# Optimization experiments

Hardware: AMD Instinct MI355X
Metric: run time of the kernel (lower is better)

The kernel has to match this reference:

```python
import jax, jax.numpy as jnp
import numpy as np
from jax import lax

B, T, K = 1024, 512, 32


def setup_inputs() -> dict:
    key = jax.random.key(0)
    k1, k2, k3 = jax.random.split(key, 3)
    labels = jax.random.randint(k1, (B, T), 0, K, dtype=jnp.int32)
    y_pred = jax.random.normal(k2, (B, T, K), dtype=jnp.float32)
    # glorot-uniform-ish transition matrix
    limit = np.sqrt(6.0 / (K + K)).astype(np.float32)
    trans = jax.random.uniform(k3, (K, K), minval=-limit, maxval=limit, dtype=jnp.float32)
    mask = jnp.ones((B, T), dtype=jnp.float32)
    return {"labels": labels, "y_pred": y_pred, "trans": trans, "mask": mask}


def crf_loss(labels, y_pred, trans, mask):
    n_tags = trans.shape[0]
    y_true = jax.nn.one_hot(labels, n_tags, dtype=y_pred.dtype)  # [B,T,K]
    y_true = y_true * mask[:, :, None]  # sequence_masking with value 0

    # --- target path score ---
    point_score = jnp.einsum('bni,bni->b', y_true, y_pred)
    trans_score = jnp.einsum('bni,ij,bnj->b', y_true[:, :-1], trans, y_true[:, 1:])
    target = point_score + trans_score

    # --- log partition via forward algorithm (logsumexp scan) ---
    alpha0 = y_pred[:, 0]  # [B,K]

    def step(alpha, xs):
        emit, m = xs  # emit: [B,K], m: [B,1]
        new = jax.nn.logsumexp(alpha[:, :, None] + trans[None], axis=1) + emit
        alpha = m * new + (1.0 - m) * alpha
        return alpha, None

    xs = (jnp.swapaxes(y_pred[:, 1:], 0, 1),          # [T-1,B,K]
          jnp.swapaxes(mask[:, 1:, None], 0, 1))      # [T-1,B,1]
    alpha, _ = lax.scan(step, alpha0, xs)
    log_norm = jax.nn.logsumexp(alpha, axis=1)  # [B]
    return log_norm - target


def reference(labels, y_pred, trans, mask):
    return crf_loss(labels, y_pred, trans, mask)
```

## Files before the change

### kernel.cpp

```cpp
#include <hip/hip_runtime.h>


#define K32 32
#define Tt  512
#define NCH 4
#define CHL 128
#define NSEG 2

typedef float  float4v __attribute__((ext_vector_type(4)));
typedef short  short8v __attribute__((ext_vector_type(8)));

__device__ inline float bf2f_lo(unsigned d) { return __uint_as_float(d << 16); }
__device__ inline float bf2f_hi(unsigned d) { return __uint_as_float(d & 0xFFFF0000u); }

__device__ inline unsigned pack_trunc(float hi, float lo) {
    return __builtin_amdgcn_perm(__float_as_uint(hi), __float_as_uint(lo), 0x07060302u);
}
__device__ inline unsigned short f2bf_rne(float x) {
    unsigned u = __float_as_uint(x);
    return (unsigned short)((u + 0x7FFFu + ((u >> 16) & 1u)) >> 16);
}

union F8 { unsigned u[4]; short8v v; };

__global__ __launch_bounds__(256, 4) void crf_chunk(
    const int*   __restrict__ labels,
    const float* __restrict__ y_pred,
    const float* __restrict__ trans,
    const float* __restrict__ mask,
    unsigned*    __restrict__ wsMT,
    float*       __restrict__ wsS,
    float*       __restrict__ wsSc)
{
    __shared__ float expAll[4][64 * 32];

    const int lane = threadIdx.x & 63;
    const int wv   = __builtin_amdgcn_readfirstlane(threadIdx.x >> 6);
    const int gw   = blockIdx.x * 4 + wv;
    const int n    = lane & 15;
    const int q    = lane >> 4;
    const int seq  = gw >> 2;
    const int c    = gw & 3;

    float* eb = &expAll[wv][0];

    const float* yp  = y_pred + (size_t)seq * Tt * K32;
    const int*   lb  = labels + (size_t)seq * Tt;
    const float* mkp = mask   + (size_t)seq * Tt;
    const int tbase = c * CHL;

    float4 pre[8];
    {
        const float4* gs = (const float4*)(yp + (size_t)tbase * K32);
#pragma unroll
        for (int jj = 0; jj < 8; ++jj) pre[jj] = gs[jj * 64 + lane];
    }

    unsigned long long mb[NSEG];
    float sc = 0.0f;
#pragma unroll
    for (int s = 0; s < NSEG; ++s) {
        const int t = tbase + s * 64 + lane;
        const int lab0 = lb[t];
        const float mlane = mkp[t];
        float scl = yp[t * K32 + lab0] * mlane;
        if (t < Tt - 1) {
            scl += trans[lab0 * K32 + lb[t + 1]] * (mlane * mkp[t + 1]);
        }
        sc += scl;
        mb[s] = __ballot(mlane != 0.0f);
    }
    if (c == 0) mb[0] &= ~1ull;
#pragma unroll
    for (int s = 1; s < 64; s <<= 1) sc += __shfl_xor(sc, s, 64);

    F8 AE0, AE1;
#pragma unroll
    for (int h = 0; h < 4; ++h) {
        const int k0 = (h < 2) ? (q * 4 + 2 * h) : (16 + q * 4 + 2 * (h - 2));
        const int k1 = k0 + 1;
        AE0.u[h] = ((unsigned)f2bf_rne(__expf(trans[k0 * K32 + n]) * 0.03125f)) |
                   (((unsigned)f2bf_rne(__expf(trans[k1 * K32 + n]) * 0.03125f)) << 16);
        AE1.u[h] = ((unsigned)f2bf_rne(__expf(trans[k0 * K32 + 16 + n]) * 0.03125f)) |
                   (((unsigned)f2bf_rne(__expf(trans[k1 * K32 + 16 + n]) * 0.03125f)) << 16);
    }

    F8 B0, B1;
#pragma unroll
    for (int h = 0; h < 4; ++h) {
        const int r0 = (h < 2) ? (q * 4 + 2 * h) : (16 + q * 4 + 2 * (h - 2));
        const int r1 = r0 + 1;
        unsigned w0 = 0, w1 = 0;
        if (r0 == n)      w0 |= 0x3F80u;
        if (r1 == n)      w0 |= 0x3F800000u;
        if (r0 == 16 + n) w1 |= 0x3F80u;
        if (r1 == 16 + n) w1 |= 0x3F800000u;
        B0.u[h] = w0;
        B1.u[h] = w1;
    }

    float Slog    = 0.0f;
    int   applied = 0;

    const int svoff0 = q * 4;
    const int svoff1 = 16 + q * 4;

    auto body = [&](int i) {
        const float4v sv0 = *(const float4v*)&eb[i * 32 + svoff0];
        const float4v sv1 = *(const float4v*)&eb[i * 32 + svoff1];

        float4v c00 = {0.f, 0.f, 0.f, 0.f}, c01 = {0.f, 0.f, 0.f, 0.f};
        float4v c10 = {0.f, 0.f, 0.f, 0.f}, c11 = {0.f, 0.f, 0.f, 0.f};
        c00 = __builtin_amdgcn_mfma_f32_16x16x32_bf16(AE0.v, B0.v, c00, 0, 0, 0);
        c01 = __builtin_amdgcn_mfma_f32_16x16x32_bf16(AE0.v, B1.v, c01, 0, 0, 0);
        c10 = __builtin_amdgcn_mfma_f32_16x16x32_bf16(AE1.v, B0.v, c10, 0, 0, 0);
        c11 = __builtin_amdgcn_mfma_f32_16x16x32_bf16(AE1.v, B1.v, c11, 0, 0, 0);

        c00 *= sv0; c01 *= sv0; c10 *= sv1; c11 *= sv1;

        if ((applied & 7) == 7) {
            const float cn = __uint_as_float(
                __builtin_amdgcn_readfirstlane(__float_as_uint(c00[0])));
            const float rs = 1.0f / cn;
            c00 *= rs; c01 *= rs; c10 *= rs; c11 *= rs;
            Slog += __logf(cn);
        }
        ++applied;

        B0.u[0] = pack_trunc(c00[1], c00[0]);
        B0.u[1] = pack_trunc(c00[3], c00[2]);
        B0.u[2] = pack_trunc(c10[1], c10[0]);
        B0.u[3] = pack_trunc(c10[3], c10[2]);
        B1.u[0] = pack_trunc(c01[1], c01[0]);
        B1.u[1] = pack_trunc(c01[3], c01[2]);
        B1.u[2] = pack_trunc(c11[1], c11[0]);
        B1.u[3] = pack_trunc(c11[3], c11[2]);
    };

    for (int seg = 0; seg < NSEG; ++seg) {
#pragma unroll
        for (int jj = 0; jj < 8; ++jj) {
            float4v e;
            e[0] = __expf(pre[jj].x); e[1] = __expf(pre[jj].y);
            e[2] = __expf(pre[jj].z); e[3] = __expf(pre[jj].w);
            *(float4v*)&eb[(jj * 64 + lane) * 4] = e;
        }
        if (seg + 1 < NSEG) {
            const float4* gs = (const float4*)(yp + (size_t)(tbase + (seg + 1) * 64) * K32);
#pragma unroll
            for (int jj = 0; jj < 8; ++jj) pre[jj] = gs[jj * 64 + lane];
        }

        const unsigned long long mbits = mb[seg];
        if (mbits == ~0ull) {
#pragma unroll 8
            for (int i = 0; i < 64; ++i) body(i);
        } else {
#pragma unroll 4
            for (int i = 0; i < 64; ++i) {
                if ((mbits >> i) & 1ull) body(i);
            }
        }
    }

    {
        unsigned* Nd = (unsigned*)eb;
        *(uint2*)&Nd[n * 20 + q * 2]            = make_uint2(B0.u[0], B0.u[1]);
        *(uint2*)&Nd[n * 20 + 8 + q * 2]        = make_uint2(B0.u[2], B0.u[3]);
        *(uint2*)&Nd[(16 + n) * 20 + q * 2]     = make_uint2(B1.u[0], B1.u[1]);
        *(uint2*)&Nd[(16 + n) * 20 + 8 + q * 2] = make_uint2(B1.u[2], B1.u[3]);
    }
    const unsigned short* Ncm = (const unsigned short*)eb;
    unsigned* md = wsMT + (size_t)gw * 512;
    for (int idx = lane; idx < 512; idx += 64) {
        const int k = idx >> 4, d = idx & 15;
        const unsigned lo = Ncm[(2 * d) * 40 + k];
        const unsigned hi = Ncm[(2 * d + 1) * 40 + k];
        md[idx] = lo | (hi << 16);
    }
    if (lane == 0) {
        wsS[gw]  = Slog + (float)applied * 3.46573590f;
        wsSc[gw] = sc;
    }
}

__global__ __launch_bounds__(64) void crf_combine(
    const float*    __restrict__ y_pred,
    const unsigned* __restrict__ wsMT,
    const float*    __restrict__ wsS,
    const float*    __restrict__ wsSc,
    float*          __restrict__ out)
{
    const int lane = threadIdx.x;
    const int h    = lane >> 5;
    const int j    = lane & 31;
    const int seq  = blockIdx.x;

    const uint4* mb = (const uint4*)(wsMT + (size_t)seq * NCH * 512);
    uint4 mA[NCH], mB[NCH];
#pragma unroll
    for (int cc = 0; cc < NCH; ++cc) {
        mA[cc] = mb[cc * 128 + j * 4 + 2 * h];
        mB[cc] = mb[cc * 128 + j * 4 + 2 * h + 1];
    }

    const float* yp = y_pred + (size_t)seq * Tt * K32;
    const float a0 = yp[j];
    const float m0 = __shfl(a0, 0, 64);
    float p = __expf(a0 - m0);
    float S = m0;

    float scs = 0.0f;
#pragma unroll
    for (int cc = 0; cc < NCH; ++cc) {
        S   += wsS[seq * NCH + cc];
        scs += wsSc[seq * NCH + cc];
    }

    const int cb = h << 4;
#pragma unroll
    for (int cc = 0; cc < NCH; ++cc) {
        const float cn = __shfl(p, 0, 64);
        const unsigned u0 = mA[cc].x, u1 = mA[cc].y, u2 = mA[cc].z, u3 = mA[cc].w;
        const unsigned u4 = mB[cc].x, u5 = mB[cc].y, u6 = mB[cc].z, u7 = mB[cc].w;
        float acc = 0.0f;
        acc = fmaf(__shfl(p, cb +  0, 64), bf2f_lo(u0), acc);
        acc = fmaf(__shfl(p, cb +  1, 64), bf2f_hi(u0), acc);
        acc = fmaf(__shfl(p, cb +  2, 64), bf2f_lo(u1), acc);
        acc = fmaf(__shfl(p, cb +  3, 64), bf2f_hi(u1), acc);
        acc = fmaf(__shfl(p, cb +  4, 64), bf2f_lo(u2), acc);
        acc = fmaf(__shfl(p, cb +  5, 64), bf2f_hi(u2), acc);
        acc = fmaf(__shfl(p, cb +  6, 64), bf2f_lo(u3), acc);
        acc = fmaf(__shfl(p, cb +  7, 64), bf2f_hi(u3), acc);
        acc = fmaf(__shfl(p, cb +  8, 64), bf2f_lo(u4), acc);
        acc = fmaf(__shfl(p, cb +  9, 64), bf2f_hi(u4), acc);
        acc = fmaf(__shfl(p, cb + 10, 64), bf2f_lo(u5), acc);
        acc = fmaf(__shfl(p, cb + 11, 64), bf2f_hi(u5), acc);
        acc = fmaf(__shfl(p, cb + 12, 64), bf2f_lo(u6), acc);
        acc = fmaf(__shfl(p, cb + 13, 64), bf2f_hi(u6), acc);
        acc = fmaf(__shfl(p, cb + 14, 64), bf2f_lo(u7), acc);
        acc = fmaf(__shfl(p, cb + 15, 64), bf2f_hi(u7), acc);
        acc += __shfl_xor(acc, 32, 64);
        p = acc * (1.0f / cn);
        S += __logf(cn);
    }

    float sp = p;
    sp += __shfl_xor(sp,  1, 64);
    sp += __shfl_xor(sp,  2, 64);
    sp += __shfl_xor(sp,  4, 64);
    sp += __shfl_xor(sp,  8, 64);
    sp += __shfl_xor(sp, 16, 64);

    if (lane == 0) {
        out[seq] = S + __logf(sp) - scs;
    }
}

extern "C" void kernel_launch(void* const* d_in, const int* in_sizes, int n_in,
                              void* d_out, int out_size, void* d_ws, size_t ws_size,
                              hipStream_t stream) {
    const int*   labels = (const int*)  d_in[0];
    const float* y_pred = (const float*)d_in[1];
    const float* trans  = (const float*)d_in[2];
    const float* mask   = (const float*)d_in[3];
    float* out = (float*)d_out;

    unsigned* wsMT = (unsigned*)d_ws;
    float* wsS  = (float*)((char*)d_ws + (size_t)1024 * NCH * 512 * 4);
    float* wsSc = wsS + 1024 * NCH;

    crf_chunk<<<1024, 256, 0, stream>>>(labels, y_pred, trans, mask, wsMT, wsS, wsSc);
    crf_combine<<<1024, 64, 0, stream>>>(y_pred, wsMT, wsS, wsSc, out);
}
```

Measured before the change: 143.0 us.

## Fuse chunk and combine kernels via shared-memory handoff within block

Merges the chunk kernel and the combine kernel into one launch. Each block now handles a single sequence: its four waves compute the four chunk transfer matrices, write them to LDS instead of global workspace, and wave 0 chains them after a block barrier. This removes a kernel launch, the global workspace round trip and the second pass over the data. In exchange, three waves sit idle during the serial combine phase.

```diff
diff --git a/kernel.cpp b/kernel.cpp
--- a/kernel.cpp
+++ b/kernel.cpp
@@ -23,24 +23,21 @@
 
 union F8 { unsigned u[4]; short8v v; };
 
-__global__ __launch_bounds__(256, 4) void crf_chunk(
+__global__ __launch_bounds__(256, 4) void crf_fused(
     const int*   __restrict__ labels,
     const float* __restrict__ y_pred,
     const float* __restrict__ trans,
     const float* __restrict__ mask,
-    unsigned*    __restrict__ wsMT,
-    float*       __restrict__ wsS,
-    float*       __restrict__ wsSc)
+    float*       __restrict__ out)
 {
-    __shared__ float expAll[4][64 * 32];
+    __shared__ float expAll[4][2048];
 
     const int lane = threadIdx.x & 63;
     const int wv   = __builtin_amdgcn_readfirstlane(threadIdx.x >> 6);
-    const int gw   = blockIdx.x * 4 + wv;
     const int n    = lane & 15;
     const int q    = lane >> 4;
-    const int seq  = gw >> 2;
-    const int c    = gw & 3;
+    const int seq  = blockIdx.x;
+    const int c    = wv;
 
     float* eb = &expAll[wv][0];
 
@@ -164,96 +161,91 @@
     }
 
     {
-        unsigned* Nd = (unsigned*)eb;
+        unsigned* Nd = (unsigned*)eb + 1024;
         *(uint2*)&Nd[n * 20 + q * 2]            = make_uint2(B0.u[0], B0.u[1]);
         *(uint2*)&Nd[n * 20 + 8 + q * 2]        = make_uint2(B0.u[2], B0.u[3]);
         *(uint2*)&Nd[(16 + n) * 20 + q * 2]     = make_uint2(B1.u[0], B1.u[1]);
         *(uint2*)&Nd[(16 + n) * 20 + 8 + q * 2] = make_uint2(B1.u[2], B1.u[3]);
     }
-    const unsigned short* Ncm = (const unsigned short*)eb;
-    unsigned* md = wsMT + (size_t)gw * 512;
-    for (int idx = lane; idx < 512; idx += 64) {
-        const int k = idx >> 4, d = idx & 15;
-        const unsigned lo = Ncm[(2 * d) * 40 + k];
-        const unsigned hi = Ncm[(2 * d + 1) * 40 + k];
-        md[idx] = lo | (hi << 16);
+    {
+        const unsigned short* Ncm = (const unsigned short*)((unsigned*)eb + 1024);
+        unsigned* md = (unsigned*)eb;
+        for (int idx = lane; idx < 512; idx += 64) {
+            const int k = idx >> 4, d = idx & 15;
+            const unsigned lo = Ncm[(2 * d) * 40 + k];
+            const unsigned hi = Ncm[(2 * d + 1) * 40 + k];
+            md[idx] = lo | (hi << 16);
+        }
     }
     if (lane == 0) {
-        wsS[gw]  = Slog + (float)applied * 3.46573590f;
-        wsSc[gw] = sc;
-    }
-}
-
-__global__ __launch_bounds__(64) void crf_combine(
-    const float*    __restrict__ y_pred,
-    const unsigned* __restrict__ wsMT,
-    const float*    __restrict__ wsS,
-    const float*    __restrict__ wsSc,
-    float*          __restrict__ out)
-{
-    const int lane = threadIdx.x;
-    const int h    = lane >> 5;
-    const int j    = lane & 31;
-    const int seq  = blockIdx.x;
-
-    const uint4* mb = (const uint4*)(wsMT + (size_t)seq * NCH * 512);
-    uint4 mA[NCH], mB[NCH];
-#pragma unroll
-    for (int cc = 0; cc < NCH; ++cc) {
-        mA[cc] = mb[cc * 128 + j * 4 + 2 * h];
-        mB[cc] = mb[cc * 128 + j * 4 + 2 * h + 1];
-    }
-
-    const float* yp = y_pred + (size_t)seq * Tt * K32;
-    const float a0 = yp[j];
-    const float m0 = __shfl(a0, 0, 64);
-    float p = __expf(a0 - m0);
-    float S = m0;
-
-    float scs = 0.0f;
-#pragma unroll
-    for (int cc = 0; cc < NCH; ++cc) {
-        S   += wsS[seq * NCH + cc];
-        scs += wsSc[seq * NCH + cc];
-    }
-
-    const int cb = h << 4;
-#pragma unroll
-    for (int cc = 0; cc < NCH; ++cc) {
-        const float cn = __shfl(p, 0, 64);
-        const unsigned u0 = mA[cc].x, u1 = mA[cc].y, u2 = mA[cc].z, u3 = mA[cc].w;
-        const unsigned u4 = mB[cc].x, u5 = mB[cc].y, u6 = mB[cc].z, u7 = mB[cc].w;
-        float acc = 0.0f;
-        acc = fmaf(__shfl(p, cb +  0, 64), bf2f_lo(u0), acc);
-        acc = fmaf(__shfl(p, cb +  1, 64), bf2f_hi(u0), acc);
-        acc = fmaf(__shfl(p, cb +  2, 64), bf2f_lo(u1), acc);
-        acc = fmaf(__shfl(p, cb +  3, 64), bf2f_hi(u1), acc);
-        acc = fmaf(__shfl(p, cb +  4, 64), bf2f_lo(u2), acc);
-        acc = fmaf(__shfl(p, cb +  5, 64), bf2f_hi(u2), acc);
-        acc = fmaf(__shfl(p, cb +  6, 64), bf2f_lo(u3), acc);
-        acc = fmaf(__shfl(p, cb +  7, 64), bf2f_hi(u3), acc);
-        acc = fmaf(__shfl(p, cb +  8, 64), bf2f_lo(u4), acc);
-        acc = fmaf(__shfl(p, cb +  9, 64), bf2f_hi(u4), acc);
-        acc = fmaf(__shfl(p, cb + 10, 64), bf2f_lo(u5), acc);
-        acc = fmaf(__shfl(p, cb + 11, 64), bf2f_hi(u5), acc);
-        acc = fmaf(__shfl(p, cb + 12, 64), bf2f_lo(u6), acc);
-        acc = fmaf(__shfl(p, cb + 13, 64), bf2f_hi(u6), acc);
-        acc = fmaf(__shfl(p, cb + 14, 64), bf2f_lo(u7), acc);
-        acc = fmaf(__shfl(p, cb + 15, 64), bf2f_hi(u7), acc);
-        acc += __shfl_xor(acc, 32, 64);
-        p = acc * (1.0f / cn);
-        S += __logf(cn);
-    }
-
-    float sp = p;
-    sp += __shfl_xor(sp,  1, 64);
-    sp += __shfl_xor(sp,  2, 64);
-    sp += __shfl_xor(sp,  4, 64);
-    sp += __shfl_xor(sp,  8, 64);
-    sp += __shfl_xor(sp, 16, 64);
-
-    if (lane == 0) {
-        out[seq] = S + __logf(sp) - scs;
+        eb[1984] = Slog + (float)applied * 3.46573590f;
+        eb[1985] = sc;
+    }
+
+    __syncthreads();
+
+    if (wv == 0) {
+        const int h = lane >> 5;
+        const int j = lane & 31;
+
+        uint4 mA[NCH], mB[NCH];
+#pragma unroll
+        for (int cc = 0; cc < NCH; ++cc) {
+            const unsigned* mt = (const unsigned*)&expAll[cc][0];
+            mA[cc] = *(const uint4*)&mt[j * 16 + 8 * h];
+            mB[cc] = *(const uint4*)&mt[j * 16 + 8 * h + 4];
+        }
+
+        const float a0 = yp[j];
+        const float m0 = __shfl(a0, 0, 64);
+        float p = __expf(a0 - m0);
+        float S = m0;
+
+        float scs = 0.0f;
+#pragma unroll
+        for (int cc = 0; cc < NCH; ++cc) {
+            S   += expAll[cc][1984];
+            scs += expAll[cc][1985];
+        }
+
+        const int cb = h << 4;
+#pragma unroll
+        for (int cc = 0; cc < NCH; ++cc) {
+            const float cn = __shfl(p, 0, 64);
+            const unsigned u0 = mA[cc].x, u1 = mA[cc].y, u2 = mA[cc].z, u3 = mA[cc].w;
+            const unsigned u4 = mB[cc].x, u5 = mB[cc].y, u6 = mB[cc].z, u7 = mB[cc].w;
+            float acc = 0.0f;
+            acc = fmaf(__shfl(p, cb +  0, 64), bf2f_lo(u0), acc);
+            acc = fmaf(__shfl(p, cb +  1, 64), bf2f_hi(u0), acc);
+            acc = fmaf(__shfl(p, cb +  2, 64), bf2f_lo(u1), acc);
+            acc = fmaf(__shfl(p, cb +  3, 64), bf2f_hi(u1), acc);
+            acc = fmaf(__shfl(p, cb +  4, 64), bf2f_lo(u2), acc);
+            acc = fmaf(__shfl(p, cb +  5, 64), bf2f_hi(u2), acc);
+            acc = fmaf(__shfl(p, cb +  6, 64), bf2f_lo(u3), acc);
+            acc = fmaf(__shfl(p, cb +  7, 64), bf2f_hi(u3), acc);
+            acc = fmaf(__shfl(p, cb +  8, 64), bf2f_lo(u4), acc);
+            acc = fmaf(__shfl(p, cb +  9, 64), bf2f_hi(u4), acc);
+            acc = fmaf(__shfl(p, cb + 10, 64), bf2f_lo(u5), acc);
+            acc = fmaf(__shfl(p, cb + 11, 64), bf2f_hi(u5), acc);
+            acc = fmaf(__shfl(p, cb + 12, 64), bf2f_lo(u6), acc);
+            acc = fmaf(__shfl(p, cb + 13, 64), bf2f_hi(u6), acc);
+            acc = fmaf(__shfl(p, cb + 14, 64), bf2f_lo(u7), acc);
+            acc = fmaf(__shfl(p, cb + 15, 64), bf2f_hi(u7), acc);
+            acc += __shfl_xor(acc, 32, 64);
+            p = acc * (1.0f / cn);
+            S += __logf(cn);
+        }
+
+        float sp = p;
+        sp += __shfl_xor(sp,  1, 64);
+        sp += __shfl_xor(sp,  2, 64);
+        sp += __shfl_xor(sp,  4, 64);
+        sp += __shfl_xor(sp,  8, 64);
+        sp += __shfl_xor(sp, 16, 64);
+
+        if (lane == 0) {
+            out[seq] = S + __logf(sp) - scs;
+        }
     }
 }
 
@@ -266,10 +258,5 @@
     const float* mask   = (const float*)d_in[3];
     float* out = (float*)d_out;
 
-    unsigned* wsMT = (unsigned*)d_ws;
-    float* wsS  = (float*)((char*)d_ws + (size_t)1024 * NCH * 512 * 4);
-    float* wsSc = wsS + 1024 * NCH;
-
-    crf_chunk<<<1024, 256, 0, stream>>>(labels, y_pred, trans, mask, wsMT, wsS, wsSc);
-    crf_combine<<<1024, 64, 0, stream>>>(y_pred, wsMT, wsS, wsSc, out);
-}
+    crf_fused<<<1024, 256, 0, stream>>>(labels, y_pred, trans, mask, out);
+}
```

After: 141.5 us. Within noise of the previous version (-1.1%).
